# Kernel tuning notes

Hardware: AMD Instinct MI355X
Metric: run time of the kernel (lower is better)

Reference implementation:

```python
import jax, jax.numpy as jnp
import numpy as np
import math

MEM_DIM = 256   # channel dim of each memory slot
FEA_DIM = 1000  # number of memory slots (softmax axis)


def setup_inputs() -> dict:
    key = jax.random.key(0)
    kx, kw = jax.random.split(key)
    x = jax.random.normal(kx, (32, 64, 64, MEM_DIM), dtype=jnp.float32)
    std = 1.0 / math.sqrt(FEA_DIM)
    weight = jax.random.uniform(kw, (FEA_DIM, MEM_DIM), dtype=jnp.float32,
                                minval=-std, maxval=std)
    return {"x": x, "weight": weight}


def reference(x, weight):
    B, H, W, C = x.shape            # C == mem_dim
    xf = x.reshape(-1, C)           # [N, C], N = B*H*W
    # distance = inputs @ weight^T -> [N, fea_dim]
    dist = jnp.einsum('nc,fc->nf', xf, weight)
    att = jax.nn.softmax(dist, axis=1)          # [N, fea_dim]
    out = jnp.einsum('nf,fc->nc', att, weight)  # [N, C]
    out = out.reshape(B, H, W, C)
    # entropy: reshape att to [B, H*W*fea_dim], mean(-a*log a) per sample
    a = att.reshape(B, -1)
    ent = jnp.mean(-a * jnp.log(a), axis=-1, keepdims=True)  # [B, 1]
    return out, ent
```

## Files before the change

kernel.cpp:

```cpp
#include <hip/hip_runtime.h>
#include <stdint.h>

typedef unsigned int u32;
typedef unsigned short u16;
typedef u32 u32x4 __attribute__((ext_vector_type(4)));
typedef float f32x4 __attribute__((ext_vector_type(4)));

#define MEM_DIM 256
#define FEA 1000
#define FPAD 1024
#define BM 128
#define NIT 32
#define NOUT 33554432

__device__ __forceinline__ u16 f2bf(float x) {
  u32 u = __builtin_bit_cast(u32, x);
  u32 r = (u + 0x7fffu + ((u >> 16) & 1u)) >> 16;
  return (u16)r;
}

__device__ __forceinline__ u32 packbf(float a, float b) {
  return (u32)f2bf(a) | ((u32)f2bf(b) << 16);
}

__device__ __forceinline__ void mfma16(f32x4& acc, u32x4 a, u32x4 b) {
  asm("v_mfma_f32_16x16x32_bf16 %0, %1, %2, %0" : "+v"(acc) : "v"(a), "v"(b));
}

#define GLOAD_LDS16(gp, lp) __builtin_amdgcn_global_load_lds( \
    (const __attribute__((address_space(1))) u32*)(gp),       \
    (__attribute__((address_space(3))) u32*)(lp), 16, 0, 0)

__global__ void prep_kernel(const float* __restrict__ W, u16* __restrict__ Wswz,
                            u16* __restrict__ Wt, float* __restrict__ entpart) {
  int f = blockIdx.x;
  int c = threadIdx.x;
  float v = (f < FEA) ? W[f * MEM_DIM + c] : 0.0f;
  u16 b = f2bf(v);
  Wswz[f * MEM_DIM + (c ^ ((f & 7) << 3))] = b;
  Wt[c * FPAD + (f ^ (((c >> 1) & 3) << 3))] = b;
  if (blockIdx.x < 4) entpart[blockIdx.x * 256 + threadIdx.x] = 0.0f;
}

__global__ __launch_bounds__(256, 2) void fused_kernel(
    const float* __restrict__ X, const u16* __restrict__ Wswz,
    const u16* __restrict__ Wt, float* __restrict__ Out,
    float* __restrict__ entpart) {
  __shared__ __attribute__((aligned(16))) char smem[65536];
  __shared__ float entw[4];
  const int tid = threadIdx.x;
  const int wave = tid >> 6;
  const int lane = tid & 63;
  const int g = lane >> 4;
  const int q = lane & 15;
  const long rowbase = (long)blockIdx.x * BM + wave * 32;

  u32x4 xf[2][8];
#pragma unroll
  for (int ms = 0; ms < 2; ++ms) {
    const float* xr = X + (rowbase + ms * 16 + q) * MEM_DIM;
#pragma unroll
    for (int kk = 0; kk < 8; ++kk) {
      const f32x4* p = (const f32x4*)(xr + kk * 32 + g * 8);
      f32x4 a = p[0], b = p[1];
      u32x4 v;
      v.x = packbf(a.x, a.y); v.y = packbf(a.z, a.w);
      v.z = packbf(b.x, b.y); v.w = packbf(b.z, b.w);
      xf[ms][kk] = v;
    }
  }

  const char* WswzB = (const char*)Wswz;
  const char* WtB = (const char*)Wt;
  auto stage = [&](int it, int buf) {
#pragma unroll
    for (int jj = 0; jj < 4; ++jj) {
      int j = wave * 4 + jj;
      GLOAD_LDS16(WswzB + (size_t)it * 16384 + j * 1024 + lane * 16,
                  smem + buf * 16384 + j * 1024);
    }
#pragma unroll
    for (int jj = 0; jj < 4; ++jj) {
      int j = wave * 4 + jj;
      GLOAD_LDS16(WtB + (size_t)it * 64 + (size_t)(16 * j + (lane >> 2)) * 2048
                      + (lane & 3) * 16,
                  smem + 32768 + buf * 16384 + j * 1024);
    }
  };

  f32x4 ot[16][2];
  f32x4 z4 = {0.f, 0.f, 0.f, 0.f};
#pragma unroll
  for (int i = 0; i < 16; ++i) { ot[i][0] = z4; ot[i][1] = z4; }
  float zz[2] = {0.f, 0.f}, tt[2] = {0.f, 0.f};

  stage(0, 0);
  asm volatile("s_waitcnt vmcnt(0)" ::: "memory");
  __syncthreads();

  for (int it = 0; it < NIT; ++it) {
    const int cur = it & 1;
    if (it + 1 < NIT) stage(it + 1, cur ^ 1);
    const char* wb = smem + cur * 16384;
    const char* wt = smem + 32768 + cur * 16384;

    f32x4 st[2][2];
    st[0][0] = z4; st[0][1] = z4; st[1][0] = z4; st[1][1] = z4;
#pragma unroll
    for (int kk = 0; kk < 8; ++kk) {
#pragma unroll
      for (int fs = 0; fs < 2; ++fs) {
        const int fl = fs * 16 + q;
        const int off = fl * 512 + ((kk * 64 + g * 16) ^ ((fl & 7) << 4));
        u32x4 wfrag = *(const u32x4*)(wb + off);
        mfma16(st[fs][0], wfrag, xf[0][kk]);
        mfma16(st[fs][1], wfrag, xf[1][kk]);
      }
    }

    const int fbase = it * 32;
    u32 pw[2][2][2];
#pragma unroll
    for (int fs = 0; fs < 2; ++fs) {
#pragma unroll
      for (int ms = 0; ms < 2; ++ms) {
        float pv[4];
#pragma unroll
        for (int r = 0; r < 4; ++r) {
          float s = st[fs][ms][r];
          int fg = fbase + fs * 16 + g * 4 + r;
          float p = (fg < FEA) ? __expf(s) : 0.0f;
          pv[r] = p;
          zz[ms] += p;
          tt[ms] += p * s;
        }
        pw[fs][ms][0] = packbf(pv[0], pv[1]);
        pw[fs][ms][1] = packbf(pv[2], pv[3]);
      }
    }

    u32x4 pfrag[2];
#pragma unroll
    for (int ms = 0; ms < 2; ++ms) {
      u32 wd[4];
#pragma unroll
      for (int w = 0; w < 4; ++w) {
        int src = ((2 * (g & 1) + (w >> 1)) << 4) | q;
        u32 v0 = (u32)__shfl((int)pw[0][ms][w & 1], src, 64);
        u32 v1 = (u32)__shfl((int)pw[1][ms][w & 1], src, 64);
        wd[w] = (g >= 2) ? v1 : v0;
      }
      u32x4 pf; pf.x = wd[0]; pf.y = wd[1]; pf.z = wd[2]; pf.w = wd[3];
      pfrag[ms] = pf;
    }

#pragma unroll
    for (int ct = 0; ct < 16; ++ct) {
      const int off = ct * 1024 + q * 64 + ((g << 4) ^ (((q >> 1) & 3) << 4));
      u32x4 wtfrag = *(const u32x4*)(wt + off);
      mfma16(ot[ct][0], wtfrag, pfrag[0]);
      mfma16(ot[ct][1], wtfrag, pfrag[1]);
    }

    asm volatile("s_waitcnt vmcnt(0)" ::: "memory");
    __syncthreads();
  }

#pragma unroll
  for (int ms = 0; ms < 2; ++ms) {
    zz[ms] += __shfl_xor(zz[ms], 16, 64);
    zz[ms] += __shfl_xor(zz[ms], 32, 64);
    tt[ms] += __shfl_xor(tt[ms], 16, 64);
    tt[ms] += __shfl_xor(tt[ms], 32, 64);
  }

  float er = 0.0f;
#pragma unroll
  for (int ms = 0; ms < 2; ++ms) er += __logf(zz[ms]) - tt[ms] / zz[ms];
#pragma unroll
  for (int d = 1; d < 64; d <<= 1) er += __shfl_xor(er, d, 64);
  if (lane == 0) entw[wave] = er * 0.25f;

#pragma unroll
  for (int ms = 0; ms < 2; ++ms) {
    float rz = 1.0f / zz[ms];
    float* orow = Out + (rowbase + ms * 16 + q) * MEM_DIM;
#pragma unroll
    for (int ct = 0; ct < 16; ++ct) {
      f32x4 v = ot[ct][ms] * rz;
      *(f32x4*)(orow + ct * 16 + g * 4) = v;
    }
  }

  __syncthreads();
  if (tid == 0) entpart[blockIdx.x] = entw[0] + entw[1] + entw[2] + entw[3];
}

__global__ void ent_final(const float* __restrict__ entpart,
                          float* __restrict__ entout) {
  int b = blockIdx.x;
  int l = threadIdx.x;
  float v = (l < 32) ? entpart[b * 32 + l] : 0.0f;
#pragma unroll
  for (int d = 1; d < 64; d <<= 1) v += __shfl_xor(v, d, 64);
  if (l == 0) entout[b] = v * (1.0f / 4096000.0f);
}

extern "C" void kernel_launch(void* const* d_in, const int* in_sizes, int n_in,
                              void* d_out, int out_size, void* d_ws, size_t ws_size,
                              hipStream_t stream) {
  (void)in_sizes; (void)n_in; (void)out_size;
  const float* X = (const float*)d_in[0];
  const float* W = (const float*)d_in[1];
  float* Out = (float*)d_out;
  u16* Wswz = (u16*)d_ws;
  u16* Wt = (u16*)((char*)d_ws + 524288);
  float* entpart = (float*)((char*)d_ws + 1048576);
  if (ws_size < 1048576 + 4096) return;
  prep_kernel<<<dim3(1024), dim3(256), 0, stream>>>(W, Wswz, Wt, entpart);
  fused_kernel<<<dim3(1024), dim3(256), 0, stream>>>(X, Wswz, Wt, Out, entpart);
  ent_final<<<dim3(32), dim3(64), 0, stream>>>(entpart, Out + NOUT);
}
```

Baseline: 182.0 us.

## Software-pipeline GEMM1 of next tile against softmax and GEMM2 of current tile

Restructures the main loop so the first GEMM for tile it+1 is issued between the softmax and the second GEMM of tile it. The two weight stages now have separate prefetch schedules, with the Wswz load running two tiles ahead. The aim is to overlap the exp/shuffle softmax work with MFMA work and shorten the dependency stalls inside each iteration. The cost is a longer prologue and epilogue, and it may raise register pressure under the 2-wave-per-SIMD launch bound.

New measurement: 223.8 us. 23.0% more time.

```diff
diff --git a/kernel.cpp b/kernel.cpp
--- a/kernel.cpp
+++ b/kernel.cpp
@@ -72,19 +72,21 @@
 
   const char* WswzB = (const char*)Wswz;
   const char* WtB = (const char*)Wt;
-  auto stage = [&](int it, int buf) {
+  auto stage_wb = [&](int T, int b) {
 #pragma unroll
     for (int jj = 0; jj < 4; ++jj) {
       int j = wave * 4 + jj;
-      GLOAD_LDS16(WswzB + (size_t)it * 16384 + j * 1024 + lane * 16,
-                  smem + buf * 16384 + j * 1024);
-    }
+      GLOAD_LDS16(WswzB + (size_t)T * 16384 + j * 1024 + lane * 16,
+                  smem + b * 16384 + j * 1024);
+    }
+  };
+  auto stage_wt = [&](int T, int b) {
 #pragma unroll
     for (int jj = 0; jj < 4; ++jj) {
       int j = wave * 4 + jj;
-      GLOAD_LDS16(WtB + (size_t)it * 64 + (size_t)(16 * j + (lane >> 2)) * 2048
+      GLOAD_LDS16(WtB + (size_t)T * 64 + (size_t)(16 * j + (lane >> 2)) * 2048
                       + (lane & 3) * 16,
-                  smem + 32768 + buf * 16384 + j * 1024);
+                  smem + 32768 + b * 16384 + j * 1024);
     }
   };
 
@@ -93,18 +95,11 @@
 #pragma unroll
   for (int i = 0; i < 16; ++i) { ot[i][0] = z4; ot[i][1] = z4; }
   float zz[2] = {0.f, 0.f}, tt[2] = {0.f, 0.f};
-
-  stage(0, 0);
-  asm volatile("s_waitcnt vmcnt(0)" ::: "memory");
-  __syncthreads();
-
-  for (int it = 0; it < NIT; ++it) {
-    const int cur = it & 1;
-    if (it + 1 < NIT) stage(it + 1, cur ^ 1);
-    const char* wb = smem + cur * 16384;
-    const char* wt = smem + 32768 + cur * 16384;
-
-    f32x4 st[2][2];
+  f32x4 st[2][2];
+  u32x4 pfrag[2];
+
+  auto gemm1 = [&](int b) {
+    const char* wb = smem + b * 16384;
     st[0][0] = z4; st[0][1] = z4; st[1][0] = z4; st[1][1] = z4;
 #pragma unroll
     for (int kk = 0; kk < 8; ++kk) {
@@ -117,7 +112,9 @@
         mfma16(st[fs][1], wfrag, xf[1][kk]);
       }
     }
-
+  };
+
+  auto softmax = [&](int it) {
     const int fbase = it * 32;
     u32 pw[2][2][2];
 #pragma unroll
@@ -138,8 +135,6 @@
         pw[fs][ms][1] = packbf(pv[2], pv[3]);
       }
     }
-
-    u32x4 pfrag[2];
 #pragma unroll
     for (int ms = 0; ms < 2; ++ms) {
       u32 wd[4];
@@ -153,7 +148,10 @@
       u32x4 pf; pf.x = wd[0]; pf.y = wd[1]; pf.z = wd[2]; pf.w = wd[3];
       pfrag[ms] = pf;
     }
-
+  };
+
+  auto gemm2 = [&](int it) {
+    const char* wt = smem + 32768 + (it & 1) * 16384;
 #pragma unroll
     for (int ct = 0; ct < 16; ++ct) {
       const int off = ct * 1024 + q * 64 + ((g << 4) ^ (((q >> 1) & 3) << 4));
@@ -161,10 +159,27 @@
       mfma16(ot[ct][0], wtfrag, pfrag[0]);
       mfma16(ot[ct][1], wtfrag, pfrag[1]);
     }
-
+  };
+
+  stage_wb(0, 0);
+  stage_wt(0, 0);
+  stage_wb(1, 1);
+  asm volatile("s_waitcnt vmcnt(0)" ::: "memory");
+  __syncthreads();
+  gemm1(0);
+  __syncthreads();
+
+  for (int it = 0; it < NIT - 1; ++it) {
+    if (it + 2 < NIT) stage_wb(it + 2, it & 1);
+    stage_wt(it + 1, (it + 1) & 1);
+    softmax(it);
+    gemm1((it + 1) & 1);
+    gemm2(it);
     asm volatile("s_waitcnt vmcnt(0)" ::: "memory");
     __syncthreads();
   }
+  softmax(NIT - 1);
+  gemm2(NIT - 1);
 
 #pragma unroll
   for (int ms = 0; ms < 2; ++ms) {
```
